# Kernel optimization log

Hardware: AMD Instinct MI355X
Metric: run time of the kernel (lower is better)

## Reference

```python
import jax, jax.numpy as jnp
import numpy as np
from jax import lax

NC = 32
EPS = 1e-12


def unfold3x3(x):
    # x: [B,C,H,W] -> [B, C*9, H*W], matching F.unfold(kernel=3, padding=1)
    B, C, H, W = x.shape
    xp = jnp.pad(x, ((0, 0), (0, 0), (1, 1), (1, 1)))
    patches = jnp.stack([xp[:, :, i:i + H, j:j + W]
                         for i in range(3) for j in range(3)], axis=2)  # [B,C,9,H,W]
    return patches.reshape(B, C * 9, H * W)


def fold3x3(u, H, W):
    # u: [B, C*9, H*W] -> [B, C, H, W], matching F.fold(kernel=3, padding=1)
    B = u.shape[0]
    C = u.shape[1] // 9
    p = u.reshape(B, C, 3, 3, H, W)
    out = jnp.zeros((B, C, H + 2, W + 2), u.dtype)
    for i in range(3):
        for j in range(3):
            out = out.at[:, :, i:i + H, j:j + W].add(p[:, :, i, j])
    return out[:, :, 1:H + 1, 1:W + 1]


def l2norm(x, axis):
    n = jnp.sqrt(jnp.sum(x * x, axis=axis, keepdims=True))
    return x / jnp.maximum(n, EPS)


def conv3x3(x, w, b):
    y = lax.conv_general_dilated(x, w, (1, 1), 'SAME',
                                 dimension_numbers=('NCHW', 'OIHW', 'NCHW'))
    return y + b[None, :, None, None]


def setup_inputs() -> dict:
    key = jax.random.key(0)
    k = jax.random.split(key, 6)
    B, C, H, W = 2, NC, 80, 80
    in_HSI = jax.random.normal(k[0], (B, C, H, W), jnp.float32)
    in_PAN = jax.random.normal(k[1], (B, C, H, W), jnp.float32)
    fan1 = 2 * C * 9
    fan2 = C * 9
    w1 = jax.random.normal(k[2], (C, 2 * C, 3, 3), jnp.float32) / np.sqrt(fan1)
    b1 = jax.random.normal(k[3], (C,), jnp.float32) * 0.01
    w2 = jax.random.normal(k[4], (C, C, 3, 3), jnp.float32) / np.sqrt(fan2)
    b2 = jax.random.normal(k[5], (C,), jnp.float32) * 0.01
    return {"in_HSI": in_HSI, "in_PAN": in_PAN, "w1": w1, "b1": b1, "w2": w2, "b2": b2}


def reference(in_HSI, in_PAN, w1, b1, w2, b2):
    B, C, H, W = in_HSI.shape
    L = H * W
    HSI_unfold = unfold3x3(in_HSI)                      # [B, C*9, L]
    PAN_unfold = unfold3x3(in_PAN)                      # [B, C*9, L]
    PAN_q = l2norm(jnp.transpose(PAN_unfold, (0, 2, 1)), axis=2)  # [B, L, C*9]
    HSI_k = l2norm(HSI_unfold, axis=1)                  # [B, C*9, L]
    R = jnp.einsum('blc,bcm->blm', PAN_q, HSI_k)        # [B, L, L]
    R_star = jnp.max(R, axis=1)                         # [B, L]
    R_arg = jnp.argmax(R, axis=1)                       # [B, L]
    # gather columns of unfold(in_PAN) selected by 1-NN indices
    T_unfold = jnp.take_along_axis(PAN_unfold, R_arg[:, None, :], axis=2)
    T_lv3 = fold3x3(T_unfold, H, W) / 9.0               # [B, C, H, W]
    S = R_star.reshape(B, 1, H, W)
    h = jax.nn.relu(conv3x3(jnp.concatenate([T_lv3, in_HSI], axis=1), w1, b1))
    res = conv3x3(h, w2, b2) * S + in_HSI
    return res
```

## Files before the change

kernel.cpp:

```cpp
#include <hip/hip_runtime.h>
#include <hip/hip_bf16.h>
#include <hip/hip_fp16.h>
#include <stdint.h>

#define HH 80
#define WW 80
#define LL 6400
#define CC 32
#define BB 2
#define COG 16
#define DELTA 0.011f
#define NT8 800

typedef __bf16 bf16x8 __attribute__((ext_vector_type(8)));
typedef float  f32x4  __attribute__((ext_vector_type(4)));

__device__ __forceinline__ int div80(int v) {
    return (int)(((unsigned)v * 52429u) >> 22);
}

__device__ __forceinline__ unsigned short f2bf(float f) {
    unsigned int u = __float_as_uint(f);
    return (unsigned short)((u + 0x7fffu + ((u >> 16) & 1u)) >> 16);
}

__device__ __forceinline__ void gload_lds16(void* g, void* l) {
    __builtin_amdgcn_global_load_lds(
        (__attribute__((address_space(1))) void*)g,
        (__attribute__((address_space(3))) void*)l, 16, 0, 0);
}

__global__ __launch_bounds__(256) void fusedunf_kernel(const float* __restrict__ HSI,
                                                       const float* __restrict__ PAN,
                                                       float* __restrict__ invH,
                                                       float* __restrict__ invP,
                                                       float* __restrict__ PANunf,
                                                       float* __restrict__ HSIunf,
                                                       char* __restrict__ Apack,
                                                       char* __restrict__ Bpack) {
    __shared__ float simg[CC][3][82];
    __shared__ float sinv[80];
    const int y = blockIdx.x, mat = blockIdx.y, b = blockIdx.z;
    const int tid = threadIdx.x;
    const float* img = (mat ? HSI : PAN) + (size_t)b * CC * LL;

    for (int i = tid; i < CC * 3; i += 256) {
        simg[i / 3][i % 3][0] = 0.f;
        simg[i / 3][i % 3][81] = 0.f;
    }
    for (int i = tid; i < CC * 3 * 80; i += 256) {
        int c = i / 240, r = i - c * 240;
        int dy = r / 80, x = r - dy * 80;
        int yy = y + dy - 1;
        float v = ((unsigned)yy < 80u) ? img[(size_t)c * LL + yy * 80 + x] : 0.f;
        simg[c][dy][x + 1] = v;
    }
    __syncthreads();

    if (tid < 80) {
        float s = 0.f;
        #pragma unroll 4
        for (int c = 0; c < CC; ++c)
            #pragma unroll
            for (int dy = 0; dy < 3; ++dy)
                #pragma unroll
                for (int dx = 0; dx < 3; ++dx) {
                    float v = simg[c][dy][tid + dx];
                    s = fmaf(v, v, s);
                }
        float inv = 1.f / fmaxf(sqrtf(s), 1e-12f);
        sinv[tid] = inv;
        (mat ? invH : invP)[b * LL + y * 80 + tid] = inv;
    }
    __syncthreads();

    {
        float* unfBase = (mat ? HSIunf : PANunf) + ((size_t)b * LL + y * 80) * 288;
        for (int i = tid; i < 5760; i += 256) {
            const int fidx = i * 4;
            const int l = fidx / 288, k = fidx - l * 288;
            float4 v;
            {
                int kk = k;     int c = kk / 9, t = kk - c * 9; v.x = simg[c][t / 3][l + t % 3];
                kk = k + 1;     c = kk / 9; t = kk - c * 9;     v.y = simg[c][t / 3][l + t % 3];
                kk = k + 2;     c = kk / 9; t = kk - c * 9;     v.z = simg[c][t / 3][l + t % 3];
                kk = k + 3;     c = kk / 9; t = kk - c * 9;     v.w = simg[c][t / 3][l + t % 3];
            }
            *(float4*)(unfBase + fidx) = v;
        }
    }

    {
        char* pk = mat ? Bpack : Apack;
        for (int i = tid; i < 2880; i += 256) {
            const int l = i / 36, g = i - l * 36;
            const float inv = sinv[l];
            unsigned short hs[8];
            #pragma unroll
            for (int jj = 0; jj < 8; ++jj) {
                int kk = g * 8 + jj;
                int c = kk / 9, t = kk - c * 9;
                hs[jj] = f2bf(simg[c][t / 3][l + t % 3] * inv);
            }
            const int q = g / 12;
            const int slot = (g % 12) ^ (l & 15);
            size_t off = ((size_t)(b * 3 + q) * LL + y * 80 + l) * 256 + slot * 16;
            uint4 hv;
            hv.x = hs[0] | ((unsigned)hs[1] << 16); hv.y = hs[2] | ((unsigned)hs[3] << 16);
            hv.z = hs[4] | ((unsigned)hs[5] << 16); hv.w = hs[6] | ((unsigned)hs[7] << 16);
            *(uint4*)(pk + off) = hv;
        }
    }
}

__global__ __launch_bounds__(256, 2) void simq_kernel(const char* __restrict__ Apack,
                                                      const char* __restrict__ Bpack,
                                                      __half* __restrict__ tileMax8) {
    __shared__ __align__(16) char Alds[2][32768];
    const int orig = blockIdx.x;
    const int xcd = orig & 7, idx = orig >> 3;
    const int wg = (xcd < 4 ? xcd * 63 : 252 + (xcd - 4) * 62) + idx;
    const int b = wg / 250;
    int rest = wg - b * 250;
    const int sp = rest / 50;
    const int mt = rest - sp * 50;

    const int tid = threadIdx.x;
    const int lane = tid & 63, w = tid >> 6;
    const int wl = w >> 1, wm = w & 1;
    const int r15 = lane & 15, h = lane >> 4;
    const char* Ab = Apack + (size_t)b * 3 * LL * 256;
    const char* Bb = Bpack + (size_t)b * 3 * LL * 256;
    const int m0 = mt * 128;
    const f32x4 fzero = {0.f, 0.f, 0.f, 0.f};

    bf16x8 bq[3][3][4];
    {
        const int rowb = m0 + wm * 64 + r15;
        #pragma unroll
        for (int c = 0; c < 3; ++c)
            #pragma unroll
            for (int ks = 0; ks < 3; ++ks)
                #pragma unroll
                for (int fm = 0; fm < 4; ++fm) {
                    const int gp = ((ks * 4 + h) ^ r15) * 16;
                    bq[c][ks][fm] = *(const bf16x8*)(Bb + ((size_t)c * LL + rowb + fm * 16) * 256 + gp);
                }
    }

    const char* gAbase = Ab + w * 8192 + lane * 16;
    char* lA0 = Alds[0] + w * 8192;
    char* lA1 = Alds[1] + w * 8192;

    {
        const char* gA = gAbase + ((size_t)(sp * 10) * 128) * 256;
        #pragma unroll
        for (int i = 0; i < 8; ++i) gload_lds16((void*)(gA + i * 1024), lA0 + i * 1024);
    }

    int cur = 0;
    #pragma unroll 1
    for (int lt = 0; lt < 10; ++lt) {
        const int l0 = (sp * 10 + lt) * 128;
        f32x4 acc[4][4];
        #pragma unroll
        for (int i = 0; i < 4; ++i)
            #pragma unroll
            for (int j = 0; j < 4; ++j) acc[i][j] = fzero;

        #pragma unroll
        for (int c = 0; c < 3; ++c) {
            if (c < 2 || lt < 9) {
                const int c2  = (c + 1) % 3;
                const int l0n = (c == 2) ? l0 + 128 : l0;
                const char* gA = gAbase + ((size_t)c2 * LL + l0n) * 256;
                char* lA = (cur ^ 1) ? lA1 : lA0;
                #pragma unroll
                for (int i = 0; i < 8; ++i) gload_lds16((void*)(gA + i * 1024), lA + i * 1024);
                asm volatile("s_waitcnt vmcnt(8)" ::: "memory");
            } else {
                asm volatile("s_waitcnt vmcnt(0)" ::: "memory");
            }
            __builtin_amdgcn_s_barrier();
            asm volatile("" ::: "memory");
            const char* lAr = Alds[cur];
            #pragma unroll
            for (int ks = 0; ks < 3; ++ks) {
                const int gp = ((ks * 4 + h) ^ r15) * 16;
                bf16x8 af[4];
                #pragma unroll
                for (int f = 0; f < 4; ++f)
                    af[f] = *(const bf16x8*)(lAr + (wl * 64 + f * 16 + r15) * 256 + gp);
                #pragma unroll
                for (int fl = 0; fl < 4; ++fl)
                    #pragma unroll
                    for (int fm = 0; fm < 4; ++fm)
                        acc[fl][fm] = __builtin_amdgcn_mfma_f32_16x16x32_bf16(
                            af[fl], bq[c][ks][fm], acc[fl][fm], 0, 0, 0);
            }
            asm volatile("s_waitcnt lgkmcnt(0)" ::: "memory");
            __builtin_amdgcn_s_barrier();
            asm volatile("" ::: "memory");
            cur ^= 1;
        }

        const int Tbase = (sp * 10 + lt) * 16 + wl * 8;
        #pragma unroll
        for (int fl = 0; fl < 4; ++fl) {
            #pragma unroll
            for (int fm = 0; fm < 4; ++fm) {
                f32x4 a = acc[fl][fm];
                float v = fmaxf(fmaxf(a[0], a[1]), fmaxf(a[2], a[3]));
                v = fmaxf(v, __shfl_xor(v, 16, 64));
                if ((h & 1) == 0) {
                    const int m = m0 + wm * 64 + fm * 16 + r15;
                    tileMax8[((size_t)b * LL + m) * NT8 + Tbase + fl * 2 + (h >> 1)] = __float2half(v);
                }
            }
        }
    }
}

__global__ __launch_bounds__(256) void scanfix_kernel(const float* __restrict__ PANunf,
                                                      const float* __restrict__ HSIunf,
                                                      const float* __restrict__ invH,
                                                      const float* __restrict__ invP,
                                                      const __half* __restrict__ tileMax8,
                                                      float* __restrict__ Sv, int* __restrict__ Sa) {
    const int gw = blockIdx.x * 4 + (threadIdx.x >> 6);
    const int lane = threadIdx.x & 63;
    const int b = gw / LL;
    const __half* tm = tileMax8 + (size_t)gw * NT8;

    float tv[13];
    #pragma unroll
    for (int i = 0; i < 13; ++i) {
        int T = i * 64 + lane;
        tv[i] = (T < NT8) ? __half2float(tm[T]) : -3.0e38f;
    }
    float v1 = tv[0];
    #pragma unroll
    for (int i = 1; i < 13; ++i) v1 = fmaxf(v1, tv[i]);
    #pragma unroll
    for (int d = 1; d < 64; d <<= 1) v1 = fmaxf(v1, __shfl_xor(v1, d, 64));
    const float th = v1 - DELTA;

    const float ihm = invH[gw];
    const int lql = lane >> 3, kq = lane & 7;

    float hreg[36];
    {
        const float4* hv4 = (const float4*)(HSIunf + (size_t)gw * 288 + kq * 36);
        #pragma unroll
        for (int j = 0; j < 9; ++j) {
            float4 v = hv4[j];
            hreg[j * 4 + 0] = v.x; hreg[j * 4 + 1] = v.y;
            hreg[j * 4 + 2] = v.z; hreg[j * 4 + 3] = v.w;
        }
    }

    float bv = -3.0e38f; int bl = 0x7fffffff;

    #pragma unroll 1
    for (int i = 0; i < 13; ++i) {
        unsigned long long mask = __ballot(tv[i] >= th);
        while (mask) {
            const int t = __ffsll((long long)mask) - 1;
            mask &= mask - 1;
            const int T = i * 64 + t;
            const int l = T * 8 + lql;
            const float4* pv4 = (const float4*)(PANunf + ((size_t)b * LL + l) * 288 + kq * 36);
            float part = 0.f;
            #pragma unroll
            for (int j = 0; j < 9; ++j) {
                float4 p = pv4[j];
                part = fmaf(p.x, hreg[j * 4 + 0], part);
                part = fmaf(p.y, hreg[j * 4 + 1], part);
                part = fmaf(p.z, hreg[j * 4 + 2], part);
                part = fmaf(p.w, hreg[j * 4 + 3], part);
            }
            part += __shfl_xor(part, 1, 64);
            part += __shfl_xor(part, 2, 64);
            part += __shfl_xor(part, 4, 64);
            const float val = part * invP[b * LL + l] * ihm;
            if (val > bv || (val == bv && l < bl)) { bv = val; bl = l; }
        }
    }
    #pragma unroll
    for (int d = 1; d < 64; d <<= 1) {
        float ov = __shfl_xor(bv, d, 64);
        int   ol = __shfl_xor(bl, d, 64);
        if (ov > bv || (ov == bv && ol < bl)) { bv = ov; bl = ol; }
    }
    if (lane == 0) { Sv[gw] = bv; Sa[gw] = bl; }
}

__global__ void tfold_kernel(const float* __restrict__ PAN, const int* __restrict__ Sa,
                             float* __restrict__ T) {
    int g = blockIdx.x * blockDim.x + threadIdx.x;
    if (g >= BB * CC * LL) return;
    int bc = g / LL, l = g - bc * LL;
    int b = bc >> 5;
    int y = div80(l), x = l - y * 80;
    const float* img = PAN + (size_t)bc * LL;
    const int* Sab = Sa + b * LL;
    float acc = 0.f;
    #pragma unroll
    for (int i = 0; i < 3; ++i) {
        int yp = y + 1 - i;
        if ((unsigned)yp >= 80u) continue;
        #pragma unroll
        for (int j = 0; j < 3; ++j) {
            int xp = x + 1 - j;
            if ((unsigned)xp >= 80u) continue;
            int a = Sab[yp * 80 + xp];
            int ya = div80(a), xa = a - ya * 80;
            int py = ya + i - 1, px = xa + j - 1;
            if ((unsigned)py < 80u && (unsigned)px < 80u) acc += img[py * 80 + px];
        }
    }
    T[g] = acc * (1.f / 9.f);
}

__global__ __launch_bounds__(256) void conv1_kernel(const float* __restrict__ T,
                                                    const float* __restrict__ HSI,
                                                    const float* __restrict__ w1,
                                                    const float* __restrict__ b1,
                                                    float* __restrict__ h) {
    __shared__ __align__(16) float wl[64][9][COG];
    const int tid = threadIdx.x;
    const int co0 = blockIdx.y * COG;
    for (int idx = tid; idx < 64 * 9 * COG; idx += 256) {
        int cog = idx & (COG - 1);
        int rest = idx >> 4;
        int cin = rest / 9, tap = rest - cin * 9;
        wl[cin][tap][cog] = w1[(co0 + cog) * (64 * 9) + cin * 9 + tap];
    }
    __syncthreads();
    const int g = blockIdx.x * 256 + tid;
    const int b = g / LL, l = g - b * LL;
    const int y = div80(l), x = l - y * 80;
    float acc[COG];
    #pragma unroll
    for (int i = 0; i < COG; ++i) acc[i] = 0.f;
    for (int cin = 0; cin < 64; ++cin) {
        const float* img = (cin < CC) ? (T + (size_t)(b * CC + cin) * LL)
                                      : (HSI + (size_t)(b * CC + (cin - CC)) * LL);
        float tap[9];
        #pragma unroll
        for (int i = 0; i < 3; ++i)
            #pragma unroll
            for (int j = 0; j < 3; ++j) {
                int yy = y + i - 1, xx = x + j - 1;
                tap[i * 3 + j] = ((unsigned)yy < 80u && (unsigned)xx < 80u) ? img[yy * 80 + xx] : 0.f;
            }
        #pragma unroll
        for (int t9 = 0; t9 < 9; ++t9) {
            #pragma unroll
            for (int q4 = 0; q4 < COG / 4; ++q4) {
                const float4 wv = *reinterpret_cast<const float4*>(&wl[cin][t9][q4 * 4]);
                acc[q4 * 4 + 0] = fmaf(tap[t9], wv.x, acc[q4 * 4 + 0]);
                acc[q4 * 4 + 1] = fmaf(tap[t9], wv.y, acc[q4 * 4 + 1]);
                acc[q4 * 4 + 2] = fmaf(tap[t9], wv.z, acc[q4 * 4 + 2]);
                acc[q4 * 4 + 3] = fmaf(tap[t9], wv.w, acc[q4 * 4 + 3]);
            }
        }
    }
    #pragma unroll
    for (int cog = 0; cog < COG; ++cog) {
        float v = acc[cog] + b1[co0 + cog];
        h[(size_t)(b * CC + co0 + cog) * LL + l] = fmaxf(v, 0.f);
    }
}

__global__ __launch_bounds__(256) void conv2_kernel(const float* __restrict__ hbuf,
                                                    const float* __restrict__ HSI,
                                                    const float* __restrict__ Sv,
                                                    const float* __restrict__ w2,
                                                    const float* __restrict__ b2,
                                                    float* __restrict__ out) {
    __shared__ __align__(16) float wl[CC][9][COG];
    const int tid = threadIdx.x;
    const int co0 = blockIdx.y * COG;
    for (int idx = tid; idx < CC * 9 * COG; idx += 256) {
        int cog = idx & (COG - 1);
        int rest = idx >> 4;
        int cin = rest / 9, tap = rest - cin * 9;
        wl[cin][tap][cog] = w2[(co0 + cog) * (CC * 9) + cin * 9 + tap];
    }
    __syncthreads();
    const int g = blockIdx.x * 256 + tid;
    const int b = g / LL, l = g - b * LL;
    const int y = div80(l), x = l - y * 80;
    float acc[COG];
    #pragma unroll
    for (int i = 0; i < COG; ++i) acc[i] = 0.f;
    for (int cin = 0; cin < CC; ++cin) {
        const float* img = hbuf + (size_t)(b * CC + cin) * LL;
        float tap[9];
        #pragma unroll
        for (int i = 0; i < 3; ++i)
            #pragma unroll
            for (int j = 0; j < 3; ++j) {
                int yy = y + i - 1, xx = x + j - 1;
                tap[i * 3 + j] = ((unsigned)yy < 80u && (unsigned)xx < 80u) ? img[yy * 80 + xx] : 0.f;
            }
        #pragma unroll
        for (int t9 = 0; t9 < 9; ++t9) {
            #pragma unroll
            for (int q4 = 0; q4 < COG / 4; ++q4) {
                const float4 wv = *reinterpret_cast<const float4*>(&wl[cin][t9][q4 * 4]);
                acc[q4 * 4 + 0] = fmaf(tap[t9], wv.x, acc[q4 * 4 + 0]);
                acc[q4 * 4 + 1] = fmaf(tap[t9], wv.y, acc[q4 * 4 + 1]);
                acc[q4 * 4 + 2] = fmaf(tap[t9], wv.z, acc[q4 * 4 + 2]);
                acc[q4 * 4 + 3] = fmaf(tap[t9], wv.w, acc[q4 * 4 + 3]);
            }
        }
    }
    const float s = Sv[b * LL + l];
    #pragma unroll
    for (int cog = 0; cog < COG; ++cog) {
        int c = co0 + cog;
        out[(size_t)(b * CC + c) * LL + l] = fmaf(acc[cog] + b2[c], s, HSI[(size_t)(b * CC + c) * LL + l]);
    }
}

extern "C" void kernel_launch(void* const* d_in, const int* in_sizes, int n_in,
                              void* d_out, int out_size, void* d_ws, size_t ws_size,
                              hipStream_t stream) {
    const float* HSI = (const float*)d_in[0];
    const float* PAN = (const float*)d_in[1];
    const float* w1  = (const float*)d_in[2];
    const float* b1  = (const float*)d_in[3];
    const float* w2  = (const float*)d_in[4];
    const float* b2  = (const float*)d_in[5];
    float* out = (float*)d_out;

    char* ws = (char*)d_ws;
    size_t off = 0;
    auto alloc = [&](size_t bytes) -> void* {
        void* p = ws + off;
        off += (bytes + 255) & ~(size_t)255;
        return p;
    };
    float* invH  = (float*)alloc((size_t)BB * LL * 4);
    float* invP  = (float*)alloc((size_t)BB * LL * 4);
    char*  Apack = (char*) alloc((size_t)BB * 3 * LL * 256);
    char*  Bpack = (char*) alloc((size_t)BB * 3 * LL * 256);
    __half* tileMax8 = (__half*)alloc((size_t)BB * LL * NT8 * 2);
    float* PANunf = (float*)alloc((size_t)BB * LL * 288 * 4);
    float* HSIunf = (float*)alloc((size_t)BB * LL * 288 * 4);
    float* Sv    = (float*)alloc((size_t)BB * LL * 4);
    int*   Sa    = (int*)  alloc((size_t)BB * LL * 4);
    float* T     = (float*)alloc((size_t)BB * CC * LL * 4);
    float* hbuf  = (float*)alloc((size_t)BB * CC * LL * 4);

    fusedunf_kernel<<<dim3(80, 2, BB), 256, 0, stream>>>(HSI, PAN, invH, invP,
                                                         PANunf, HSIunf, Apack, Bpack);
    simq_kernel<<<dim3(500), 256, 0, stream>>>(Apack, Bpack, tileMax8);
    scanfix_kernel<<<dim3(BB * LL / 4), 256, 0, stream>>>(PANunf, HSIunf, invH, invP, tileMax8, Sv, Sa);
    tfold_kernel<<<dim3((BB * CC * LL + 255) / 256), 256, 0, stream>>>(PAN, Sa, T);
    conv1_kernel<<<dim3(BB * LL / 256, CC / COG), 256, 0, stream>>>(T, HSI, w1, b1, hbuf);
    conv2_kernel<<<dim3(BB * LL / 256, CC / COG), 256, 0, stream>>>(hbuf, HSI, Sv, w2, b2, out);
}
```

Before: 221.0 us.

## Add hierarchical tile-max pruning, drop LDS staging in simq, halve conv output group

simq_kernel now reads A fragments straight from global memory instead of double-buffering them through LDS with global_load_lds and barriers. It also writes a coarser 64-column tile max alongside the 8-column one. scanfix first scans the 100 coarse maxima, then descends into the 8-column sub-tiles only for coarse tiles above threshold, which cuts per-row header reads and shrinks the candidate search. scanfix also gets an XCD-aware block swizzle, and the conv kernels drop from 16 to 8 output channels per block to raise parallelism. The risks are more global load latency in the MFMA loop and an extra output array to write.

```diff
diff --git a/kernel.cpp b/kernel.cpp
--- a/kernel.cpp
+++ b/kernel.cpp
@@ -8,7 +8,7 @@
 #define LL 6400
 #define CC 32
 #define BB 2
-#define COG 16
+#define COG 8
 #define DELTA 0.011f
 #define NT8 800
 
@@ -22,12 +22,6 @@
 __device__ __forceinline__ unsigned short f2bf(float f) {
     unsigned int u = __float_as_uint(f);
     return (unsigned short)((u + 0x7fffu + ((u >> 16) & 1u)) >> 16);
-}
-
-__device__ __forceinline__ void gload_lds16(void* g, void* l) {
-    __builtin_amdgcn_global_load_lds(
-        (__attribute__((address_space(1))) void*)g,
-        (__attribute__((address_space(3))) void*)l, 16, 0, 0);
 }
 
 __global__ __launch_bounds__(256) void fusedunf_kernel(const float* __restrict__ HSI,
@@ -115,8 +109,8 @@
 
 __global__ __launch_bounds__(256, 2) void simq_kernel(const char* __restrict__ Apack,
                                                       const char* __restrict__ Bpack,
-                                                      __half* __restrict__ tileMax8) {
-    __shared__ __align__(16) char Alds[2][32768];
+                                                      __half* __restrict__ tileMax8,
+                                                      __half* __restrict__ tileMax64) {
     const int orig = blockIdx.x;
     const int xcd = orig & 7, idx = orig >> 3;
     const int wg = (xcd < 4 ? xcd * 63 : 252 + (xcd - 4) * 62) + idx;
@@ -134,6 +128,10 @@
     const int m0 = mt * 128;
     const f32x4 fzero = {0.f, 0.f, 0.f, 0.f};
 
+    int gp[3];
+    #pragma unroll
+    for (int ks = 0; ks < 3; ++ks) gp[ks] = ((ks * 4 + h) ^ r15) * 16;
+
     bf16x8 bq[3][3][4];
     {
         const int rowb = m0 + wm * 64 + r15;
@@ -142,26 +140,16 @@
             #pragma unroll
             for (int ks = 0; ks < 3; ++ks)
                 #pragma unroll
-                for (int fm = 0; fm < 4; ++fm) {
-                    const int gp = ((ks * 4 + h) ^ r15) * 16;
-                    bq[c][ks][fm] = *(const bf16x8*)(Bb + ((size_t)c * LL + rowb + fm * 16) * 256 + gp);
-                }
-    }
-
-    const char* gAbase = Ab + w * 8192 + lane * 16;
-    char* lA0 = Alds[0] + w * 8192;
-    char* lA1 = Alds[1] + w * 8192;
-
-    {
-        const char* gA = gAbase + ((size_t)(sp * 10) * 128) * 256;
-        #pragma unroll
-        for (int i = 0; i < 8; ++i) gload_lds16((void*)(gA + i * 1024), lA0 + i * 1024);
-    }
-
-    int cur = 0;
+                for (int fm = 0; fm < 4; ++fm)
+                    bq[c][ks][fm] = *(const bf16x8*)(Bb + ((size_t)c * LL + rowb + fm * 16) * 256 + gp[ks]);
+    }
+
+    const char* Abase = Ab + (size_t)(wl * 64 + r15) * 256;
+
     #pragma unroll 1
     for (int lt = 0; lt < 10; ++lt) {
         const int l0 = (sp * 10 + lt) * 128;
+        const char* Alt = Abase + (size_t)l0 * 256;
         f32x4 acc[4][4];
         #pragma unroll
         for (int i = 0; i < 4; ++i)
@@ -170,27 +158,12 @@
 
         #pragma unroll
         for (int c = 0; c < 3; ++c) {
-            if (c < 2 || lt < 9) {
-                const int c2  = (c + 1) % 3;
-                const int l0n = (c == 2) ? l0 + 128 : l0;
-                const char* gA = gAbase + ((size_t)c2 * LL + l0n) * 256;
-                char* lA = (cur ^ 1) ? lA1 : lA0;
-                #pragma unroll
-                for (int i = 0; i < 8; ++i) gload_lds16((void*)(gA + i * 1024), lA + i * 1024);
-                asm volatile("s_waitcnt vmcnt(8)" ::: "memory");
-            } else {
-                asm volatile("s_waitcnt vmcnt(0)" ::: "memory");
-            }
-            __builtin_amdgcn_s_barrier();
-            asm volatile("" ::: "memory");
-            const char* lAr = Alds[cur];
             #pragma unroll
             for (int ks = 0; ks < 3; ++ks) {
-                const int gp = ((ks * 4 + h) ^ r15) * 16;
                 bf16x8 af[4];
                 #pragma unroll
                 for (int f = 0; f < 4; ++f)
-                    af[f] = *(const bf16x8*)(lAr + (wl * 64 + f * 16 + r15) * 256 + gp);
+                    af[f] = *(const bf16x8*)(Alt + ((size_t)c * LL + f * 16) * 256 + gp[ks]);
                 #pragma unroll
                 for (int fl = 0; fl < 4; ++fl)
                     #pragma unroll
@@ -198,25 +171,29 @@
                         acc[fl][fm] = __builtin_amdgcn_mfma_f32_16x16x32_bf16(
                             af[fl], bq[c][ks][fm], acc[fl][fm], 0, 0, 0);
             }
-            asm volatile("s_waitcnt lgkmcnt(0)" ::: "memory");
-            __builtin_amdgcn_s_barrier();
-            asm volatile("" ::: "memory");
-            cur ^= 1;
-        }
-
-        const int Tbase = (sp * 10 + lt) * 16 + wl * 8;
-        #pragma unroll
-        for (int fl = 0; fl < 4; ++fl) {
-            #pragma unroll
-            for (int fm = 0; fm < 4; ++fm) {
+        }
+
+        const int T64 = (sp * 10 + lt) * 2 + wl;
+        #pragma unroll
+        for (int fm = 0; fm < 4; ++fm) {
+            float m4[4];
+            #pragma unroll
+            for (int fl = 0; fl < 4; ++fl) {
                 f32x4 a = acc[fl][fm];
-                float v = fmaxf(fmaxf(a[0], a[1]), fmaxf(a[2], a[3]));
-                v = fmaxf(v, __shfl_xor(v, 16, 64));
-                if ((h & 1) == 0) {
-                    const int m = m0 + wm * 64 + fm * 16 + r15;
-                    tileMax8[((size_t)b * LL + m) * NT8 + Tbase + fl * 2 + (h >> 1)] = __float2half(v);
-                }
-            }
+                m4[fl] = fmaxf(fmaxf(a[0], a[1]), fmaxf(a[2], a[3]));
+            }
+            const int m = m0 + wm * 64 + fm * 16 + r15;
+            #pragma unroll
+            for (int fl = 0; fl < 4; ++fl) {
+                float v = fmaxf(m4[fl], __shfl_xor(m4[fl], 16, 64));
+                if ((h & 1) == 0)
+                    tileMax8[((size_t)b * LL + m) * NT8 + T64 * 8 + fl * 2 + (h >> 1)] = __float2half(v);
+            }
+            float vA = fmaxf(fmaxf(m4[0], m4[1]), fmaxf(m4[2], m4[3]));
+            vA = fmaxf(vA, __shfl_xor(vA, 16, 64));
+            vA = fmaxf(vA, __shfl_xor(vA, 32, 64));
+            if (h == 0)
+                tileMax64[((size_t)b * LL + m) * 100 + T64] = __float2half(vA);
         }
     }
 }
@@ -226,21 +203,23 @@
                                                       const float* __restrict__ invH,
                                                       const float* __restrict__ invP,
                                                       const __half* __restrict__ tileMax8,
+                                                      const __half* __restrict__ tileMax64,
                                                       float* __restrict__ Sv, int* __restrict__ Sa) {
-    const int gw = blockIdx.x * 4 + (threadIdx.x >> 6);
+    const int orig = blockIdx.x;
+    const int swz = (orig & 7) * 400 + (orig >> 3);
+    const int gw = swz * 4 + (threadIdx.x >> 6);
     const int lane = threadIdx.x & 63;
     const int b = gw / LL;
-    const __half* tm = tileMax8 + (size_t)gw * NT8;
-
-    float tv[13];
-    #pragma unroll
-    for (int i = 0; i < 13; ++i) {
+    const __half* tm64 = tileMax64 + (size_t)gw * 100;
+    const __half* tm8  = tileMax8  + (size_t)gw * NT8;
+
+    float t64[2];
+    #pragma unroll
+    for (int i = 0; i < 2; ++i) {
         int T = i * 64 + lane;
-        tv[i] = (T < NT8) ? __half2float(tm[T]) : -3.0e38f;
-    }
-    float v1 = tv[0];
-    #pragma unroll
-    for (int i = 1; i < 13; ++i) v1 = fmaxf(v1, tv[i]);
+        t64[i] = (T < 100) ? __half2float(tm64[T]) : -3.0e38f;
+    }
+    float v1 = fmaxf(t64[0], t64[1]);
     #pragma unroll
     for (int d = 1; d < 64; d <<= 1) v1 = fmaxf(v1, __shfl_xor(v1, d, 64));
     const float th = v1 - DELTA;
@@ -262,28 +241,35 @@
     float bv = -3.0e38f; int bl = 0x7fffffff;
 
     #pragma unroll 1
-    for (int i = 0; i < 13; ++i) {
-        unsigned long long mask = __ballot(tv[i] >= th);
+    for (int i = 0; i < 2; ++i) {
+        unsigned long long mask = __ballot(t64[i] >= th);
         while (mask) {
             const int t = __ffsll((long long)mask) - 1;
             mask &= mask - 1;
-            const int T = i * 64 + t;
-            const int l = T * 8 + lql;
-            const float4* pv4 = (const float4*)(PANunf + ((size_t)b * LL + l) * 288 + kq * 36);
-            float part = 0.f;
-            #pragma unroll
-            for (int j = 0; j < 9; ++j) {
-                float4 p = pv4[j];
-                part = fmaf(p.x, hreg[j * 4 + 0], part);
-                part = fmaf(p.y, hreg[j * 4 + 1], part);
-                part = fmaf(p.z, hreg[j * 4 + 2], part);
-                part = fmaf(p.w, hreg[j * 4 + 3], part);
-            }
-            part += __shfl_xor(part, 1, 64);
-            part += __shfl_xor(part, 2, 64);
-            part += __shfl_xor(part, 4, 64);
-            const float val = part * invP[b * LL + l] * ihm;
-            if (val > bv || (val == bv && l < bl)) { bv = val; bl = l; }
+            const int T64 = i * 64 + t;
+            float s8 = __half2float(tm8[T64 * 8 + (lane & 7)]);
+            unsigned sub = (unsigned)(__ballot(s8 >= th) & 0xffull);
+            while (sub) {
+                const int j = __ffs(sub) - 1;
+                sub &= sub - 1;
+                const int T = T64 * 8 + j;
+                const int l = T * 8 + lql;
+                const float4* pv4 = (const float4*)(PANunf + ((size_t)b * LL + l) * 288 + kq * 36);
+                float part = 0.f;
+                #pragma unroll
+                for (int jj = 0; jj < 9; ++jj) {
+                    float4 p = pv4[jj];
+                    part = fmaf(p.x, hreg[jj * 4 + 0], part);
+                    part = fmaf(p.y, hreg[jj * 4 + 1], part);
+                    part = fmaf(p.z, hreg[jj * 4 + 2], part);
+                    part = fmaf(p.w, hreg[jj * 4 + 3], part);
+                }
+                part += __shfl_xor(part, 1, 64);
+                part += __shfl_xor(part, 2, 64);
+                part += __shfl_xor(part, 4, 64);
+                const float val = part * invP[b * LL + l] * ihm;
+                if (val > bv || (val == bv && l < bl)) { bv = val; bl = l; }
+            }
         }
     }
     #pragma unroll
@@ -332,7 +318,7 @@
     const int co0 = blockIdx.y * COG;
     for (int idx = tid; idx < 64 * 9 * COG; idx += 256) {
         int cog = idx & (COG - 1);
-        int rest = idx >> 4;
+        int rest = idx >> 3;
         int cin = rest / 9, tap = rest - cin * 9;
         wl[cin][tap][cog] = w1[(co0 + cog) * (64 * 9) + cin * 9 + tap];
     }
@@ -356,14 +342,16 @@
             }
         #pragma unroll
         for (int t9 = 0; t9 < 9; ++t9) {
-            #pragma unroll
-            for (int q4 = 0; q4 < COG / 4; ++q4) {
-                const float4 wv = *reinterpret_cast<const float4*>(&wl[cin][t9][q4 * 4]);
-                acc[q4 * 4 + 0] = fmaf(tap[t9], wv.x, acc[q4 * 4 + 0]);
-                acc[q4 * 4 + 1] = fmaf(tap[t9], wv.y, acc[q4 * 4 + 1]);
-                acc[q4 * 4 + 2] = fmaf(tap[t9], wv.z, acc[q4 * 4 + 2]);
-                acc[q4 * 4 + 3] = fmaf(tap[t9], wv.w, acc[q4 * 4 + 3]);
-            }
+            const float4 wa = *reinterpret_cast<const float4*>(&wl[cin][t9][0]);
+            const float4 wb = *reinterpret_cast<const float4*>(&wl[cin][t9][4]);
+            acc[0] = fmaf(tap[t9], wa.x, acc[0]);
+            acc[1] = fmaf(tap[t9], wa.y, acc[1]);
+            acc[2] = fmaf(tap[t9], wa.z, acc[2]);
+            acc[3] = fmaf(tap[t9], wa.w, acc[3]);
+            acc[4] = fmaf(tap[t9], wb.x, acc[4]);
+            acc[5] = fmaf(tap[t9], wb.y, acc[5]);
+            acc[6] = fmaf(tap[t9], wb.z, acc[6]);
+            acc[7] = fmaf(tap[t9], wb.w, acc[7]);
         }
     }
     #pragma unroll
@@ -384,7 +372,7 @@
     const int co0 = blockIdx.y * COG;
     for (int idx = tid; idx < CC * 9 * COG; idx += 256) {
         int cog = idx & (COG - 1);
-        int rest = idx >> 4;
+        int rest = idx >> 3;
         int cin = rest / 9, tap = rest - cin * 9;
         wl[cin][tap][cog] = w2[(co0 + cog) * (CC * 9) + cin * 9 + tap];
     }
@@ -407,14 +395,16 @@
             }
         #pragma unroll
         for (int t9 = 0; t9 < 9; ++t9) {
-            #pragma unroll
-            for (int q4 = 0; q4 < COG / 4; ++q4) {
-                const float4 wv = *reinterpret_cast<const float4*>(&wl[cin][t9][q4 * 4]);
-                acc[q4 * 4 + 0] = fmaf(tap[t9], wv.x, acc[q4 * 4 + 0]);
-                acc[q4 * 4 + 1] = fmaf(tap[t9], wv.y, acc[q4 * 4 + 1]);
-                acc[q4 * 4 + 2] = fmaf(tap[t9], wv.z, acc[q4 * 4 + 2]);
-                acc[q4 * 4 + 3] = fmaf(tap[t9], wv.w, acc[q4 * 4 + 3]);
-            }
+            const float4 wa = *reinterpret_cast<const float4*>(&wl[cin][t9][0]);
+            const float4 wb = *reinterpret_cast<const float4*>(&wl[cin][t9][4]);
+            acc[0] = fmaf(tap[t9], wa.x, acc[0]);
+            acc[1] = fmaf(tap[t9], wa.y, acc[1]);
+            acc[2] = fmaf(tap[t9], wa.z, acc[2]);
+            acc[3] = fmaf(tap[t9], wa.w, acc[3]);
+            acc[4] = fmaf(tap[t9], wb.x, acc[4]);
+            acc[5] = fmaf(tap[t9], wb.y, acc[5]);
+            acc[6] = fmaf(tap[t9], wb.z, acc[6]);
+            acc[7] = fmaf(tap[t9], wb.w, acc[7]);
         }
     }
     const float s = Sv[b * LL + l];
@@ -447,7 +437,8 @@
     float* invP  = (float*)alloc((size_t)BB * LL * 4);
     char*  Apack = (char*) alloc((size_t)BB * 3 * LL * 256);
     char*  Bpack = (char*) alloc((size_t)BB * 3 * LL * 256);
-    __half* tileMax8 = (__half*)alloc((size_t)BB * LL * NT8 * 2);
+    __half* tileMax8  = (__half*)alloc((size_t)BB * LL * NT8 * 2);
+    __half* tileMax64 = (__half*)alloc((size_t)BB * LL * 100 * 2);
     float* PANunf = (float*)alloc((size_t)BB * LL * 288 * 4);
     float* HSIunf = (float*)alloc((size_t)BB * LL * 288 * 4);
     float* Sv    = (float*)alloc((size_t)BB * LL * 4);
@@ -457,8 +448,9 @@
 
     fusedunf_kernel<<<dim3(80, 2, BB), 256, 0, stream>>>(HSI, PAN, invH, invP,
                                                          PANunf, HSIunf, Apack, Bpack);
-    simq_kernel<<<dim3(500), 256, 0, stream>>>(Apack, Bpack, tileMax8);
-    scanfix_kernel<<<dim3(BB * LL / 4), 256, 0, stream>>>(PANunf, HSIunf, invH, invP, tileMax8, Sv, Sa);
+    simq_kernel<<<dim3(500), 256, 0, stream>>>(Apack, Bpack, tileMax8, tileMax64);
+    scanfix_kernel<<<dim3(BB * LL / 4), 256, 0, stream>>>(PANunf, HSIunf, invH, invP,
+                                                          tileMax8, tileMax64, Sv, Sa);
     tfold_kernel<<<dim3((BB * CC * LL + 255) / 256), 256, 0, stream>>>(PAN, Sa, T);
     conv1_kernel<<<dim3(BB * LL / 256, CC / COG), 256, 0, stream>>>(T, HSI, w1, b1, hbuf);
     conv2_kernel<<<dim3(BB * LL / 256, CC / COG), 256, 0, stream>>>(hbuf, HSI, Sv, w2, b2, out);
```

New measurement: 272.6 us. 23.4% more time.
